# Kernel tuning notes

Measured on AMD Instinct MI355X. Metric: run time of the kernel, lower is better.

Reference implementation:

```python
import jax, jax.numpy as jnp
import numpy as np

H, W = 512, 512
G = 8192
ALPHA_THRESH = 1.0 / 255.0        # meta_f32[0]
TRANS_THRESH = 1.0e-4             # meta_f32[1]
ALPHA_CAP = 0.99                  # meta_f32[6]
BG = jnp.zeros((3,), dtype=jnp.float32)  # config.background


def setup_inputs() -> dict:
    key = jax.random.key(0)
    ks = jax.random.split(key, 7)
    mx = jax.random.uniform(ks[0], (G,), minval=0.0, maxval=float(W))
    my = jax.random.uniform(ks[1], (G,), minval=0.0, maxval=float(H))
    means2d = jnp.stack([mx, my], axis=-1)
    # Build valid conics (inverse 2x2 covariances) from random rotation + scales
    theta = jax.random.uniform(ks[2], (G,), minval=0.0, maxval=2.0 * np.pi)
    s = jax.random.uniform(ks[3], (G, 2), minval=2.0, maxval=12.0)  # px stddevs
    ct, st = jnp.cos(theta), jnp.sin(theta)
    v1, v2 = s[:, 0] ** 2, s[:, 1] ** 2
    ca = ct * ct * v1 + st * st * v2
    cb = ct * st * (v1 - v2)
    cc = st * st * v1 + ct * ct * v2
    det = ca * cc - cb * cb
    conics = jnp.stack([cc / det, -cb / det, ca / det], axis=-1)  # [G,3] = (a,b,c)
    colors = jax.random.uniform(ks[4], (G, 3))
    opacities = jax.random.uniform(ks[5], (G,))
    depths = jax.random.uniform(ks[6], (G,), minval=0.1, maxval=100.0)
    return {"means2d": means2d, "conics": conics, "colors": colors,
            "opacities": opacities, "depths": depths}


def reference(means2d, conics, colors, opacities, depths):
    # Stable front-to-back depth sort (mirrors perm = argsort(depths, stable))
    perm = jnp.argsort(depths, stable=True)
    m = means2d[perm]
    cn = conics[perm]
    col = colors[perm]
    op = opacities[perm]
    a, b, c = cn[:, 0], cn[:, 1], cn[:, 2]
    px = jnp.arange(W, dtype=means2d.dtype) + 0.5  # pixel centers

    def row(y):
        py = y.astype(means2d.dtype) + 0.5
        dx = px[:, None] - m[None, :, 0]          # [W,G]
        dy = py - m[:, 1]                          # [G]
        sigma = 0.5 * (a * dx * dx + c * dy * dy) + b * dx * dy  # [W,G]
        alpha = jnp.minimum(ALPHA_CAP, op * jnp.exp(-sigma))
        alpha = jnp.where((sigma < 0) | (alpha < ALPHA_THRESH), 0.0, alpha)
        # exclusive cumulative transmittance along depth order
        Tprev = jnp.cumprod(1.0 - alpha, axis=-1)
        Tprev = jnp.concatenate([jnp.ones((W, 1), alpha.dtype), Tprev[:, :-1]], axis=-1)
        # early-termination: splats seen after T drops below threshold contribute 0
        wgt = alpha * Tprev * (Tprev >= TRANS_THRESH)  # [W,G]
        rgb = wgt @ col                                 # [W,3]
        t_rem = 1.0 - wgt.sum(axis=-1)                  # remaining transmittance
        return rgb + t_rem[:, None] * BG

    return jax.lax.map(row, jnp.arange(H))  # [H,W,3]
```

## Files before the change

### kernel.cpp

```cpp
#include <hip/hip_runtime.h>

#define G 8192
#define IMG_W 512
#define IMG_H 512
#define TILE 16
#define NTX (IMG_W / TILE)
#define NTY (IMG_H / TILE)
#define BLK 256
#define CAP 1024
#define ALPHA_THRESH (1.0f/255.0f)
#define ALPHA_CAP 0.99f
#define TRANS_THRESH 1e-4f

__global__ __launch_bounds__(BLK)
void range_kernel(const float* __restrict__ means2d,
                  const float* __restrict__ conics,
                  const float* __restrict__ opac,
                  unsigned int* __restrict__ ranges)
{
    int g = blockIdx.x * BLK + threadIdx.x;
    if (g >= G) return;
    float op = opac[g];
    unsigned int packed = 0xFFu;
    if (op * 255.0f >= 1.0f) {
        float smax = __logf(op * 255.0f);
        float a = conics[3*g], b = conics[3*g+1], c = conics[3*g+2];
        float det = fmaxf(a * c - b * b, 1e-12f);
        float rx = sqrtf(fmaxf(2.0f * smax * c / det, 0.0f)) * 1.0001f + 0.01f;
        float ry = sqrtf(fmaxf(2.0f * smax * a / det, 0.0f)) * 1.0001f + 0.01f;
        float mx = means2d[2*g], my = means2d[2*g+1];
        int txmin = (int)ceilf ((mx - rx - 15.5f) * 0.0625f);
        int txmax = (int)floorf((mx + rx -  0.5f) * 0.0625f);
        int tymin = (int)ceilf ((my - ry - 15.5f) * 0.0625f);
        int tymax = (int)floorf((my + ry -  0.5f) * 0.0625f);
        if (!(txmax < 0 || txmin > NTX-1 || tymax < 0 || tymin > NTY-1 ||
              txmin > txmax || tymin > tymax)) {
            txmin = max(txmin, 0); txmax = min(txmax, NTX-1);
            tymin = max(tymin, 0); tymax = min(tymax, NTY-1);
            packed = (unsigned)txmin | ((unsigned)txmax << 8)
                   | ((unsigned)tymin << 16) | ((unsigned)tymax << 24);
        }
    }
    ranges[g] = packed;
}

__device__ __forceinline__ int hitp(unsigned p, unsigned btx, unsigned bty)
{
    return (btx >= (p & 0xffu)) & (btx <= ((p >> 8) & 0xffu)) &
           (bty >= ((p >> 16) & 0xffu)) & (bty <= (p >> 24));
}

__global__ __launch_bounds__(BLK)
void tile_kernel(const unsigned int* __restrict__ ranges,
                 const float* __restrict__ depths,
                 const float* __restrict__ means2d,
                 const float* __restrict__ conics,
                 const float* __restrict__ colors,
                 const float* __restrict__ opac,
                 float*       __restrict__ out)
{
    __shared__ unsigned short slist[CAP];
    __shared__ unsigned long long keys[CAP];
    __shared__ int woff[4];
    __shared__ float4 sq0[BLK];
    __shared__ float4 sq1[BLK];
    __shared__ float  sq2[BLK];

    const int tx = threadIdx.x, ty = threadIdx.y;
    const int t = ty * TILE + tx;
    const int lane = t & 63, w = t >> 6;
    const unsigned btx = blockIdx.x, bty = blockIdx.y;

    const uint4* r4 = (const uint4*)ranges;
    const int wbase = w * (G / 4);
    uint4 rv[8];
    #pragma unroll
    for (int i = 0; i < 8; ++i)
        rv[i] = r4[(wbase >> 2) + i * 64 + lane];

    int cnt = 0;
    #pragma unroll
    for (int i = 0; i < 8; ++i)
        cnt += hitp(rv[i].x, btx, bty) + hitp(rv[i].y, btx, bty)
             + hitp(rv[i].z, btx, bty) + hitp(rv[i].w, btx, bty);
    #pragma unroll
    for (int d = 1; d < 64; d <<= 1) cnt += __shfl_xor(cnt, d);
    if (lane == 0) woff[w] = cnt;
    __syncthreads();

    int offs = 0;
    for (int ww = 0; ww < w; ++ww) offs += woff[ww];
    const int N = min(woff[0] + woff[1] + woff[2] + woff[3], CAP);

    const unsigned long long lt = (1ull << lane) - 1ull;
    #pragma unroll
    for (int i = 0; i < 8; ++i) {
        int gbase = wbase + i * 256 + lane * 4;
        int h0 = hitp(rv[i].x, btx, bty), h1 = hitp(rv[i].y, btx, bty);
        int h2 = hitp(rv[i].z, btx, bty), h3 = hitp(rv[i].w, btx, bty);
        unsigned long long m0 = __ballot(h0), m1 = __ballot(h1);
        unsigned long long m2 = __ballot(h2), m3 = __ballot(h3);
        int pos = offs + __popcll(m0 & lt) + __popcll(m1 & lt)
                       + __popcll(m2 & lt) + __popcll(m3 & lt);
        if (h0) { if (pos < CAP) slist[pos] = (unsigned short)(gbase    ); pos++; }
        if (h1) { if (pos < CAP) slist[pos] = (unsigned short)(gbase + 1); pos++; }
        if (h2) { if (pos < CAP) slist[pos] = (unsigned short)(gbase + 2); pos++; }
        if (h3) { if (pos < CAP) slist[pos] = (unsigned short)(gbase + 3); pos++; }
        offs += __popcll(m0) + __popcll(m1) + __popcll(m2) + __popcll(m3);
    }
    __syncthreads();

    for (int i = t; i < N; i += BLK) {
        unsigned idx = slist[i];
        keys[i] = ((unsigned long long)__float_as_uint(depths[idx]) << 13)
                | (unsigned long long)idx;
    }
    __syncthreads();
    for (int i = t; i < N; i += BLK) {
        unsigned long long ke = keys[i];
        int r = 0;
        #pragma unroll 4
        for (int j = 0; j < N; ++j) r += (keys[j] < ke);
        slist[r] = (unsigned short)(ke & 0x1fffull);
    }
    __syncthreads();

    const float px = (float)(blockIdx.x * TILE + tx) + 0.5f;
    const float py = (float)(blockIdx.y * TILE + ty) + 0.5f;
    float T = 1.0f, accr = 0.0f, accg = 0.0f, accb = 0.0f;
    bool done = false;

    for (int base = 0; base < N; base += BLK) {
        int n = min(BLK, N - base);
        float4 v0 = make_float4(0.f, 0.f, 0.f, 0.f);
        float4 v1 = make_float4(0.f, 0.f, 0.f, 0.f);
        float  v2 = 0.f;
        if (t < n) {
            int idx = slist[base + t];
            v0 = make_float4(means2d[2*idx], means2d[2*idx+1],
                             conics[3*idx], conics[3*idx+1]);
            v1 = make_float4(conics[3*idx+2], opac[idx],
                             colors[3*idx], colors[3*idx+1]);
            v2 = colors[3*idx+2];
        }
        sq0[t] = v0; sq1[t] = v1; sq2[t] = v2;
        __syncthreads();

        if (!done) {
            int n4 = (n + 3) & ~3;
            for (int i = 0; i < n4 && !done; i += 4) {
                #pragma unroll
                for (int u = 0; u < 4; ++u) {
                    float4 q0 = sq0[i + u];
                    float4 q1 = sq1[i + u];
                    float  bl = sq2[i + u];
                    float dx = px - q0.x;
                    float dy = py - q0.y;
                    float sigma = 0.5f * (q0.z*dx*dx + q1.x*dy*dy)
                                + q0.w*dx*dy;
                    float al = q1.y * __expf(-sigma);
                    bool ok = (sigma >= 0.0f) && (al >= ALPHA_THRESH);
                    al = ok ? fminf(al, ALPHA_CAP) : 0.0f;
                    float wgt = al * T;
                    accr = fmaf(wgt, q1.z, accr);
                    accg = fmaf(wgt, q1.w, accg);
                    accb = fmaf(wgt, bl,   accb);
                    T *= (1.0f - al);
                }
                if (T < TRANS_THRESH) done = true;
            }
        }
        if (__syncthreads_and((int)done)) break;
    }

    const int o = ((blockIdx.y * TILE + ty) * IMG_W + blockIdx.x * TILE + tx) * 3;
    out[o]     = accr;
    out[o + 1] = accg;
    out[o + 2] = accb;
}

extern "C" void kernel_launch(void* const* d_in, const int* in_sizes, int n_in,
                              void* d_out, int out_size, void* d_ws, size_t ws_size,
                              hipStream_t stream)
{
    const float* means2d = (const float*)d_in[0];
    const float* conics  = (const float*)d_in[1];
    const float* colors  = (const float*)d_in[2];
    const float* opac    = (const float*)d_in[3];
    const float* depths  = (const float*)d_in[4];
    float* out = (float*)d_out;
    unsigned int* ranges = (unsigned int*)d_ws;

    range_kernel<<<G / BLK, BLK, 0, stream>>>(means2d, conics, opac, ranges);
    tile_kernel<<<dim3(NTX, NTY), dim3(TILE, TILE), 0, stream>>>(
        ranges, depths, means2d, conics, colors, opac, out);
}
```

Baseline: 89.88 us.

## Split tile rasterizer into binning kernel and per-wave raster kernel

```diff
diff --git a/kernel.cpp b/kernel.cpp
--- a/kernel.cpp
+++ b/kernel.cpp
@@ -11,6 +11,11 @@
 #define ALPHA_THRESH (1.0f/255.0f)
 #define ALPHA_CAP 0.99f
 #define TRANS_THRESH 1e-4f
+
+#define WS_RANGES 0
+#define WS_COUNTS (32 * 1024)
+#define WS_AB     (1 << 20)
+#define WS_BLUE   (WS_AB + (32 << 20))
 
 __global__ __launch_bounds__(BLK)
 void range_kernel(const float* __restrict__ means2d,
@@ -51,25 +56,24 @@
 }
 
 __global__ __launch_bounds__(BLK)
-void tile_kernel(const unsigned int* __restrict__ ranges,
-                 const float* __restrict__ depths,
-                 const float* __restrict__ means2d,
-                 const float* __restrict__ conics,
-                 const float* __restrict__ colors,
-                 const float* __restrict__ opac,
-                 float*       __restrict__ out)
+void bin_kernel(const unsigned int* __restrict__ ranges,
+                const float* __restrict__ depths,
+                const float* __restrict__ means2d,
+                const float* __restrict__ conics,
+                const float* __restrict__ colors,
+                const float* __restrict__ opac,
+                float4* __restrict__ ab,
+                float*  __restrict__ blue,
+                int*    __restrict__ counts)
 {
     __shared__ unsigned short slist[CAP];
     __shared__ unsigned long long keys[CAP];
     __shared__ int woff[4];
-    __shared__ float4 sq0[BLK];
-    __shared__ float4 sq1[BLK];
-    __shared__ float  sq2[BLK];
-
-    const int tx = threadIdx.x, ty = threadIdx.y;
-    const int t = ty * TILE + tx;
+
+    const int t = threadIdx.x;
     const int lane = t & 63, w = t >> 6;
     const unsigned btx = blockIdx.x, bty = blockIdx.y;
+    const int tile = bty * NTX + btx;
 
     const uint4* r4 = (const uint4*)ranges;
     const int wbase = w * (G / 4);
@@ -125,55 +129,71 @@
     }
     __syncthreads();
 
-    const float px = (float)(blockIdx.x * TILE + tx) + 0.5f;
-    const float py = (float)(blockIdx.y * TILE + ty) + 0.5f;
+    const int N4 = (N + 3) & ~3;
+    const long long base = (long long)tile * CAP;
+    for (int i = t; i < N4; i += BLK) {
+        float4 a0 = make_float4(0.f, 0.f, 0.f, 0.f);
+        float4 b0 = make_float4(0.f, 0.f, 0.f, 0.f);
+        float  bl = 0.f;
+        if (i < N) {
+            int idx = slist[i];
+            a0 = make_float4(means2d[2*idx], means2d[2*idx+1],
+                             conics[3*idx], conics[3*idx+1]);
+            b0 = make_float4(conics[3*idx+2], opac[idx],
+                             colors[3*idx], colors[3*idx+1]);
+            bl = colors[3*idx+2];
+        }
+        ab[(base + i) * 2]     = a0;
+        ab[(base + i) * 2 + 1] = b0;
+        blue[base + i] = bl;
+    }
+    if (t == 0) counts[tile] = N4;
+}
+
+__global__ __launch_bounds__(64)
+void raster_kernel(const float4* __restrict__ ab,
+                   const float*  __restrict__ blue,
+                   const int*    __restrict__ counts,
+                   float*        __restrict__ out)
+{
+    const int tx_tile = blockIdx.x >> 2;
+    const int z       = blockIdx.x & 3;
+    const int ty_tile = blockIdx.y;
+    const int tile    = ty_tile * NTX + tx_tile;
+    const int lane    = threadIdx.x;
+
+    const int x = tx_tile * TILE + (lane & 15);
+    const int y = ty_tile * TILE + z * 4 + (lane >> 4);
+    const float px = (float)x + 0.5f;
+    const float py = (float)y + 0.5f;
+
+    const int N4 = counts[tile];
+    const long long base = (long long)tile * CAP;
+
     float T = 1.0f, accr = 0.0f, accg = 0.0f, accb = 0.0f;
-    bool done = false;
-
-    for (int base = 0; base < N; base += BLK) {
-        int n = min(BLK, N - base);
-        float4 v0 = make_float4(0.f, 0.f, 0.f, 0.f);
-        float4 v1 = make_float4(0.f, 0.f, 0.f, 0.f);
-        float  v2 = 0.f;
-        if (t < n) {
-            int idx = slist[base + t];
-            v0 = make_float4(means2d[2*idx], means2d[2*idx+1],
-                             conics[3*idx], conics[3*idx+1]);
-            v1 = make_float4(conics[3*idx+2], opac[idx],
-                             colors[3*idx], colors[3*idx+1]);
-            v2 = colors[3*idx+2];
+
+    for (int i = 0; i < N4; i += 4) {
+        #pragma unroll
+        for (int u = 0; u < 4; ++u) {
+            float4 q0 = ab[(base + i + u) * 2];
+            float4 q1 = ab[(base + i + u) * 2 + 1];
+            float  bl = blue[base + i + u];
+            float dx = px - q0.x;
+            float dy = py - q0.y;
+            float sigma = 0.5f * (q0.z*dx*dx + q1.x*dy*dy) + q0.w*dx*dy;
+            float al = q1.y * __expf(-sigma);
+            bool ok = (sigma >= 0.0f) && (al >= ALPHA_THRESH);
+            al = ok ? fminf(al, ALPHA_CAP) : 0.0f;
+            float wgt = al * T;
+            accr = fmaf(wgt, q1.z, accr);
+            accg = fmaf(wgt, q1.w, accg);
+            accb = fmaf(wgt, bl,   accb);
+            T *= (1.0f - al);
         }
-        sq0[t] = v0; sq1[t] = v1; sq2[t] = v2;
-        __syncthreads();
-
-        if (!done) {
-            int n4 = (n + 3) & ~3;
-            for (int i = 0; i < n4 && !done; i += 4) {
-                #pragma unroll
-                for (int u = 0; u < 4; ++u) {
-                    float4 q0 = sq0[i + u];
-                    float4 q1 = sq1[i + u];
-                    float  bl = sq2[i + u];
-                    float dx = px - q0.x;
-                    float dy = py - q0.y;
-                    float sigma = 0.5f * (q0.z*dx*dx + q1.x*dy*dy)
-                                + q0.w*dx*dy;
-                    float al = q1.y * __expf(-sigma);
-                    bool ok = (sigma >= 0.0f) && (al >= ALPHA_THRESH);
-                    al = ok ? fminf(al, ALPHA_CAP) : 0.0f;
-                    float wgt = al * T;
-                    accr = fmaf(wgt, q1.z, accr);
-                    accg = fmaf(wgt, q1.w, accg);
-                    accb = fmaf(wgt, bl,   accb);
-                    T *= (1.0f - al);
-                }
-                if (T < TRANS_THRESH) done = true;
-            }
-        }
-        if (__syncthreads_and((int)done)) break;
-    }
-
-    const int o = ((blockIdx.y * TILE + ty) * IMG_W + blockIdx.x * TILE + tx) * 3;
+        if (T < TRANS_THRESH) break;
+    }
+
+    const int o = (y * IMG_W + x) * 3;
     out[o]     = accr;
     out[o + 1] = accg;
     out[o + 2] = accb;
@@ -189,9 +209,15 @@
     const float* opac    = (const float*)d_in[3];
     const float* depths  = (const float*)d_in[4];
     float* out = (float*)d_out;
-    unsigned int* ranges = (unsigned int*)d_ws;
+
+    char* ws = (char*)d_ws;
+    unsigned int* ranges = (unsigned int*)(ws + WS_RANGES);
+    int*          counts = (int*)         (ws + WS_COUNTS);
+    float4*       ab     = (float4*)      (ws + WS_AB);
+    float*        blue   = (float*)       (ws + WS_BLUE);
 
     range_kernel<<<G / BLK, BLK, 0, stream>>>(means2d, conics, opac, ranges);
-    tile_kernel<<<dim3(NTX, NTY), dim3(TILE, TILE), 0, stream>>>(
-        ranges, depths, means2d, conics, colors, opac, out);
-}
+    bin_kernel<<<dim3(NTX, NTY), BLK, 0, stream>>>(
+        ranges, depths, means2d, conics, colors, opac, ab, blue, counts);
+    raster_kernel<<<dim3(NTX * 4, NTY), 64, 0, stream>>>(ab, blue, counts, out);
+}
```

Result: slower. 116.7 us (+29.8%).
